# Optimization experiments

Hardware: AMD Instinct MI355X
Metric: run time of the kernel (lower is better)

## Reference

```python
import jax, jax.numpy as jnp
import numpy as np

D = 256
H = 256
B = 128
T = 512


def _init_cell(key, input_size, hidden_size):
    K = 1.0 / np.sqrt(hidden_size)
    k1, k2, k3, k4 = jax.random.split(key, 4)
    u = lambda k, shape: jax.random.uniform(k, shape, jnp.float32, -K, K)
    return (u(k1, (3 * hidden_size, input_size)),
            u(k2, (3 * hidden_size, hidden_size)),
            u(k3, (3 * hidden_size,)),
            u(k4, (3 * hidden_size,)))


def setup_inputs() -> dict:
    key = jax.random.key(0)
    kx, kf, kb = jax.random.split(key, 3)
    x = jax.random.normal(kx, (B, T, D), dtype=jnp.float32)
    w_ih_fw, w_hh_fw, b_ih_fw, b_hh_fw = _init_cell(kf, D, H)
    w_ih_bw, w_hh_bw, b_ih_bw, b_hh_bw = _init_cell(kb, D, H)
    return {
        "x": x,
        "w_ih_fw": w_ih_fw, "w_hh_fw": w_hh_fw, "b_ih_fw": b_ih_fw, "b_hh_fw": b_hh_fw,
        "w_ih_bw": w_ih_bw, "w_hh_bw": w_hh_bw, "b_ih_bw": b_ih_bw, "b_hh_bw": b_hh_bw,
    }


def _gru_scan(x_tbd, w_ih, w_hh, b_ih, b_hh):
    # x_tbd: [T, B, D]; returns outputs [T, B, H] and final h [B, H]
    h0 = jnp.zeros((x_tbd.shape[1], H), dtype=x_tbd.dtype)

    def step(h, x_t):
        xT = x_t @ w_ih.T + b_ih          # [B, 3H]
        hT = h @ w_hh.T + b_hh            # [B, 3H]
        s = jax.nn.sigmoid(xT + hT)
        r = s[:, :H]
        z = s[:, H:2 * H]
        n = jnp.tanh(xT[:, 2 * H:] + r * hT[:, 2 * H:])
        h_new = (1.0 - z) * n + z * h
        return h_new, h_new

    h_last, outs = jax.lax.scan(step, h0, x_tbd)
    return outs, h_last


def reference(x, w_ih_fw, w_hh_fw, b_ih_fw, b_hh_fw,
              w_ih_bw, w_hh_bw, b_ih_bw, b_hh_bw):
    x_tbd = jnp.swapaxes(x, 0, 1)                         # [T, B, D]
    outs_fw, h_fw = _gru_scan(x_tbd, w_ih_fw, w_hh_fw, b_ih_fw, b_hh_fw)
    outs_bw_rev, h_bw = _gru_scan(x_tbd[::-1], w_ih_bw, w_hh_bw, b_ih_bw, b_hh_bw)
    outs_bw = outs_bw_rev[::-1]
    outputs = jnp.concatenate([outs_fw, outs_bw], axis=-1)  # [T, B, 2H]
    outputs = jnp.swapaxes(outputs, 0, 1)                   # [B, T, 2H]
    return outputs, h_fw, h_bw
```

## Files before the change

kernel.cpp:

```cpp
#include <hip/hip_runtime.h>
#include <stdint.h>
#include <stddef.h>

#define T_ 512
#define B_ 128
#define D_ 256
#define H_ 256
#define NR 768
#define OUT_MAIN 33554432ull
#define XT_STRIDE 12288
#define HB 280

typedef __attribute__((ext_vector_type(4))) float f32x4;
typedef __attribute__((ext_vector_type(8))) short s16x8;

__device__ __forceinline__ unsigned short f2bf(float f) {
    union { float f; uint32_t u; } v; v.f = f;
    return (unsigned short)((v.u + 0x7FFFu + ((v.u >> 16) & 1u)) >> 16);
}
__device__ __forceinline__ float bf2f(unsigned short h) {
    union { uint32_t u; float f; } v; v.u = ((uint32_t)h) << 16;
    return v.f;
}
__device__ __forceinline__ float sigm(float x) {
    return __builtin_amdgcn_rcpf(1.f + __expf(-x));
}
__device__ __forceinline__ float tanh_(float x) {
    float e = __expf(2.f * x);
    return 1.f - 2.f * __builtin_amdgcn_rcpf(e + 1.f);
}
__device__ __forceinline__ s16x8 pack8(const float* f) {
    union { s16x8 v; unsigned short u[8]; } p;
#pragma unroll
    for (int i = 0; i < 8; ++i) p.u[i] = f2bf(f[i]);
    return p.v;
}

__global__ void k_convert(const float* __restrict__ wf, const float* __restrict__ wb,
                          unsigned short* __restrict__ dst) {
    int i = blockIdx.x * blockDim.x + threadIdx.x;
    const int n = NR * D_;
    if (i < n) dst[i] = f2bf(wf[i]);
    else if (i < 2 * n) dst[i] = f2bf(wb[i - n]);
}

__global__ __launch_bounds__(512, 2) void k_xgemm(
    const float* __restrict__ x, const unsigned short* __restrict__ wbf,
    const float* __restrict__ bih_f, const float* __restrict__ bhh_f,
    const float* __restrict__ bih_b, const float* __restrict__ bhh_b,
    unsigned short* __restrict__ XT)
{
    __shared__ __align__(16) unsigned short lds_a[64 * 72];
    const int tid = threadIdx.x;
    const int lane = tid & 63, wn = tid >> 6;
    const int t = blockIdx.x;
    const int dir = blockIdx.y >> 1, mh = blockIdx.y & 1;

    f32x4 acc[4][6];
#pragma unroll
    for (int m = 0; m < 4; ++m)
#pragma unroll
        for (int n = 0; n < 6; ++n) acc[m][n] = (f32x4){0.f, 0.f, 0.f, 0.f};

    for (int kb = 0; kb < 4; ++kb) {
        if (kb) __syncthreads();
        {
            int row = tid >> 3, seg = tid & 7;
            const float* src = x + ((size_t)(mh * 64 + row) * T_ + t) * D_ + kb * 64 + seg * 8;
            float fv[8];
            *(f32x4*)&fv[0] = *(const f32x4*)(src);
            *(f32x4*)&fv[4] = *(const f32x4*)(src + 4);
            *(s16x8*)&lds_a[row * 72 + seg * 8] = pack8(fv);
        }
        __syncthreads();
#pragma unroll
        for (int kt = 0; kt < 2; ++kt) {
            s16x8 av[4];
#pragma unroll
            for (int mt = 0; mt < 4; ++mt) {
                int r = mt * 16 + (lane & 15);
                av[mt] = *(const s16x8*)&lds_a[r * 72 + kt * 32 + (lane >> 4) * 8];
            }
#pragma unroll
            for (int nt = 0; nt < 6; ++nt) {
                int c = dir * NR + wn * 96 + nt * 16 + (lane & 15);
                s16x8 bv = *(const s16x8*)(wbf + (size_t)c * D_ + kb * 64 + kt * 32 + (lane >> 4) * 8);
#pragma unroll
                for (int mt = 0; mt < 4; ++mt)
                    acc[mt][nt] = __builtin_amdgcn_mfma_f32_16x16x32_bf16(av[mt], bv, acc[mt][nt], 0, 0, 0);
            }
        }
    }
    const float* bih = dir ? bih_b : bih_f;
    const float* bhh = dir ? bhh_b : bhh_f;
#pragma unroll
    for (int nt = 0; nt < 6; ++nt) {
        const int cw = wn * 96 + nt * 16 + (lane & 15);
        const int gate = cw >> 8, j = cw & 255;
        const int jt = (j >> 4) & 1;
        const int rtid = (j >> 5) * 64 + (((lane >> 4)) << 4) + (j & 15);
        float bias = bih[cw] + (cw < 512 ? bhh[cw] : 0.f);
#pragma unroll
        for (int mt = 0; mt < 4; ++mt) {
#pragma unroll
            for (int q = 0; q < 4; ++q) {
                int rr = mh * 64 + mt * 16 + (lane >> 4) * 4 + q;
                int bgrp = rr >> 4;
                int v = (jt * 4 + q) * 3 + gate;
                XT[((size_t)(dir * 8 + bgrp) * T_ + t) * XT_STRIDE + (size_t)rtid * 24 + v]
                    = f2bf(acc[mt][nt][q] + bias);
            }
        }
    }
}

template<int P>
__device__ __forceinline__ void gru_step(
    int s, int dir, int b0, int tid, int lane, int wid,
    const unsigned short* __restrict__ XTw, float* __restrict__ out,
    unsigned short* hb, const s16x8 (&fB)[6][8], float bhn0, float bhn1,
    s16x8 (&CUR)[3], s16x8 (&NXT)[3])
{
    const int t  = dir ? (T_ - 1 - s) : s;
    const int sn = (s < T_ - 1) ? s + 1 : s;
    const int tn = dir ? (T_ - 1 - sn) : sn;
    {
        const s16x8* p = (const s16x8*)(XTw + (size_t)tn * XT_STRIDE) + (size_t)tid * 3;
        NXT[0] = p[0]; NXT[1] = p[1]; NXT[2] = p[2];
    }
    const unsigned short* hr = hb + P * (16 * HB);
    unsigned short*       hw = hb + (P ^ 1) * (16 * HB);

    f32x4 acc[6];
#pragma unroll
    for (int n = 0; n < 6; ++n) acc[n] = (f32x4){0.f, 0.f, 0.f, 0.f};
#pragma unroll
    for (int k0 = 0; k0 < 8; ++k0) {
        s16x8 a = *(const s16x8*)&hr[(lane & 15) * HB + k0 * 32 + (lane >> 4) * 8];
#pragma unroll
        for (int nt = 0; nt < 6; ++nt)
            acc[nt] = __builtin_amdgcn_mfma_f32_16x16x32_bf16(a, fB[nt][k0], acc[nt], 0, 0, 0);
    }
#pragma unroll
    for (int jt = 0; jt < 2; ++jt) {
        const int j = 32 * wid + jt * 16 + (lane & 15);
        const float bn = jt ? bhn1 : bhn0;
#pragma unroll
        for (int q = 0; q < 4; ++q) {
            const int row = (lane >> 4) * 4 + q;
            const int v = (jt * 4 + q) * 3;
            float xr = bf2f((unsigned short)CUR[(v + 0) >> 3][(v + 0) & 7]);
            float xz = bf2f((unsigned short)CUR[(v + 1) >> 3][(v + 1) & 7]);
            float xn = bf2f((unsigned short)CUR[(v + 2) >> 3][(v + 2) & 7]);
            float hv = bf2f(hr[row * HB + j]);
            float rg = sigm(acc[jt][q] + xr);
            float zg = sigm(acc[2 + jt][q] + xz);
            float ng = tanh_(xn + rg * (acc[4 + jt][q] + bn));
            float hnew = ng + zg * (hv - ng);
            hw[row * HB + j] = f2bf(hnew);
            size_t off = ((size_t)(b0 + row) << 18) + ((size_t)t << 9) + (size_t)dir * 256 + j;
            out[off] = hnew;
            if (s == T_ - 1)
                out[OUT_MAIN + (size_t)dir * B_ * H_ + (size_t)(b0 + row) * H_ + j] = hnew;
        }
    }
    __builtin_amdgcn_sched_barrier(0);
    asm volatile("s_waitcnt lgkmcnt(0)");
    __builtin_amdgcn_s_barrier();
    __builtin_amdgcn_sched_barrier(0);
}

__global__ __launch_bounds__(512, 2) void k_recur(
    const float* __restrict__ whh_f, const float* __restrict__ whh_b,
    const float* __restrict__ bhh_f, const float* __restrict__ bhh_b,
    const unsigned short* __restrict__ XT,
    float* __restrict__ out)
{
    __shared__ __align__(16) unsigned short hb[2 * 16 * HB];
    const int tid = threadIdx.x, lane = tid & 63, wid = tid >> 6;
    const int bid = blockIdx.x;
    const int dir = bid >> 3, b0 = (bid & 7) * 16;
    const float* whh = dir ? whh_b : whh_f;
    const float* bhh = dir ? bhh_b : bhh_f;

    s16x8 fB[6][8];
#pragma unroll
    for (int g = 0; g < 3; ++g) {
#pragma unroll
        for (int half = 0; half < 2; ++half) {
            int nt = 2 * g + half;
            int cb = g * 256 + 32 * wid + half * 16;
#pragma unroll
            for (int k0 = 0; k0 < 8; ++k0) {
                const float* sp = whh + (size_t)(cb + (lane & 15)) * H_ + k0 * 32 + (lane >> 4) * 8;
                float fv[8];
                *(f32x4*)&fv[0] = *(const f32x4*)(sp);
                *(f32x4*)&fv[4] = *(const f32x4*)(sp + 4);
                fB[nt][k0] = pack8(fv);
            }
        }
    }
    const float bhn0 = bhh[512 + 32 * wid + (lane & 15)];
    const float bhn1 = bhh[512 + 32 * wid + 16 + (lane & 15)];

    for (int i = tid; i < 16 * HB / 2; i += 512) ((uint32_t*)hb)[i] = 0;
    __syncthreads();

    const unsigned short* XTw = XT + (size_t)(dir * 8 + (bid & 7)) * T_ * XT_STRIDE;
    s16x8 XA[3], XB[3];
    {
        const int t0 = dir ? (T_ - 1) : 0;
        const s16x8* p = (const s16x8*)(XTw + (size_t)t0 * XT_STRIDE) + (size_t)tid * 3;
        XA[0] = p[0]; XA[1] = p[1]; XA[2] = p[2];
    }
#pragma unroll 1
    for (int s = 0; s < T_; s += 2) {
        gru_step<0>(s,     dir, b0, tid, lane, wid, XTw, out, hb, fB, bhn0, bhn1, XA, XB);
        gru_step<1>(s + 1, dir, b0, tid, lane, wid, XTw, out, hb, fB, bhn0, bhn1, XB, XA);
    }
}

extern "C" void kernel_launch(void* const* d_in, const int* in_sizes, int n_in,
                              void* d_out, int out_size, void* d_ws, size_t ws_size,
                              hipStream_t stream) {
    const float* x     = (const float*)d_in[0];
    const float* wih_f = (const float*)d_in[1];
    const float* whh_f = (const float*)d_in[2];
    const float* bih_f = (const float*)d_in[3];
    const float* bhh_f = (const float*)d_in[4];
    const float* wih_b = (const float*)d_in[5];
    const float* whh_b = (const float*)d_in[6];
    const float* bih_b = (const float*)d_in[7];
    const float* bhh_b = (const float*)d_in[8];
    float* out = (float*)d_out;

    unsigned short* wbf = (unsigned short*)d_ws;
    unsigned short* XT  = (unsigned short*)((char*)d_ws + 786432);

    k_convert<<<dim3(768), dim3(512), 0, stream>>>(wih_f, wih_b, wbf);
    k_xgemm<<<dim3(512, 4), dim3(512), 0, stream>>>(x, wbf, bih_f, bhh_f, bih_b, bhh_b, XT);
    k_recur<<<dim3(16), dim3(512), 0, stream>>>(whh_f, whh_b, bhh_f, bhh_b, XT, out);
}
```

Before: 1.695 ms.

## Retile input GEMM to 128 rows and streamline recurrent step addressing

The input-projection GEMM now gives each block all 128 batch rows and a 384-column slice, with 8 waves split 2x4. Each weight fragment is therefore fetched once for all rows instead of once per 64-row half. In the recurrent kernel, output offsets are precomputed per thread, XT words are unpacked via 32-bit lanes, and the bf16 conversion uses the hardware v_cvt_pk_bf16_f32 instruction. This trims per-step ALU and address work on the serial critical path. The bf16 rounding now comes from the hardware instruction instead of the hand-written routine, so results could differ slightly.

```diff
diff --git a/kernel.cpp b/kernel.cpp
--- a/kernel.cpp
+++ b/kernel.cpp
@@ -13,6 +13,7 @@
 
 typedef __attribute__((ext_vector_type(4))) float f32x4;
 typedef __attribute__((ext_vector_type(8))) short s16x8;
+typedef __attribute__((ext_vector_type(4))) uint32_t u32x4;
 
 __device__ __forceinline__ unsigned short f2bf(float f) {
     union { float f; uint32_t u; } v; v.f = f;
@@ -21,6 +22,17 @@
 __device__ __forceinline__ float bf2f(unsigned short h) {
     union { uint32_t u; float f; } v; v.u = ((uint32_t)h) << 16;
     return v.f;
+}
+__device__ __forceinline__ float lo16(uint32_t w) {
+    union { uint32_t u; float f; } v; v.u = w << 16; return v.f;
+}
+__device__ __forceinline__ float hi16(uint32_t w) {
+    union { uint32_t u; float f; } v; v.u = w & 0xffff0000u; return v.f;
+}
+__device__ __forceinline__ uint32_t cvt1bf(float x) {
+    uint32_t r;
+    asm("v_cvt_pk_bf16_f32 %0, %1, %2" : "=v"(r) : "v"(x), "v"(x));
+    return r;
 }
 __device__ __forceinline__ float sigm(float x) {
     return __builtin_amdgcn_rcpf(1.f + __expf(-x));
@@ -50,11 +62,12 @@
     const float* __restrict__ bih_b, const float* __restrict__ bhh_b,
     unsigned short* __restrict__ XT)
 {
-    __shared__ __align__(16) unsigned short lds_a[64 * 72];
+    __shared__ __align__(16) unsigned short lds_a[128 * 72];
     const int tid = threadIdx.x;
-    const int lane = tid & 63, wn = tid >> 6;
+    const int lane = tid & 63, wid = tid >> 6;
+    const int wm = wid >> 2, wn = wid & 3;
     const int t = blockIdx.x;
-    const int dir = blockIdx.y >> 1, mh = blockIdx.y & 1;
+    const int cblk = blockIdx.y * 384;
 
     f32x4 acc[4][6];
 #pragma unroll
@@ -65,12 +78,15 @@
     for (int kb = 0; kb < 4; ++kb) {
         if (kb) __syncthreads();
         {
-            int row = tid >> 3, seg = tid & 7;
-            const float* src = x + ((size_t)(mh * 64 + row) * T_ + t) * D_ + kb * 64 + seg * 8;
-            float fv[8];
-            *(f32x4*)&fv[0] = *(const f32x4*)(src);
-            *(f32x4*)&fv[4] = *(const f32x4*)(src + 4);
-            *(s16x8*)&lds_a[row * 72 + seg * 8] = pack8(fv);
+            int row = tid >> 2, seg = tid & 3;
+            const float* src = x + ((size_t)row * T_ + t) * D_ + kb * 64 + seg * 16;
+            float fv[16];
+            *(f32x4*)&fv[0]  = *(const f32x4*)(src);
+            *(f32x4*)&fv[4]  = *(const f32x4*)(src + 4);
+            *(f32x4*)&fv[8]  = *(const f32x4*)(src + 8);
+            *(f32x4*)&fv[12] = *(const f32x4*)(src + 12);
+            *(s16x8*)&lds_a[row * 72 + seg * 16]     = pack8(&fv[0]);
+            *(s16x8*)&lds_a[row * 72 + seg * 16 + 8] = pack8(&fv[8]);
         }
         __syncthreads();
 #pragma unroll
@@ -78,37 +94,39 @@
             s16x8 av[4];
 #pragma unroll
             for (int mt = 0; mt < 4; ++mt) {
-                int r = mt * 16 + (lane & 15);
+                int r = wm * 64 + mt * 16 + (lane & 15);
                 av[mt] = *(const s16x8*)&lds_a[r * 72 + kt * 32 + (lane >> 4) * 8];
             }
 #pragma unroll
             for (int nt = 0; nt < 6; ++nt) {
-                int c = dir * NR + wn * 96 + nt * 16 + (lane & 15);
-                s16x8 bv = *(const s16x8*)(wbf + (size_t)c * D_ + kb * 64 + kt * 32 + (lane >> 4) * 8);
+                int c = cblk + wn * 96 + nt * 16 + (lane & 15);
+                const unsigned short* bs = wbf + (size_t)c * D_ + kb * 64 + kt * 32 + (lane >> 4) * 8;
+                s16x8 bv = *(const s16x8*)bs;
 #pragma unroll
                 for (int mt = 0; mt < 4; ++mt)
                     acc[mt][nt] = __builtin_amdgcn_mfma_f32_16x16x32_bf16(av[mt], bv, acc[mt][nt], 0, 0, 0);
             }
         }
     }
+    const int dir = blockIdx.y >> 1;
     const float* bih = dir ? bih_b : bih_f;
     const float* bhh = dir ? bhh_b : bhh_f;
 #pragma unroll
     for (int nt = 0; nt < 6; ++nt) {
-        const int cw = wn * 96 + nt * 16 + (lane & 15);
+        const int cw = (blockIdx.y & 1) * 384 + wn * 96 + nt * 16 + (lane & 15);
         const int gate = cw >> 8, j = cw & 255;
         const int jt = (j >> 4) & 1;
-        const int rtid = (j >> 5) * 64 + (((lane >> 4)) << 4) + (j & 15);
+        const int wl = (j >> 5) * 64 + (j & 15);
         float bias = bih[cw] + (cw < 512 ? bhh[cw] : 0.f);
 #pragma unroll
         for (int mt = 0; mt < 4; ++mt) {
 #pragma unroll
             for (int q = 0; q < 4; ++q) {
-                int rr = mh * 64 + mt * 16 + (lane >> 4) * 4 + q;
-                int bgrp = rr >> 4;
-                int v = (jt * 4 + q) * 3 + gate;
-                XT[((size_t)(dir * 8 + bgrp) * T_ + t) * XT_STRIDE + (size_t)rtid * 24 + v]
-                    = f2bf(acc[mt][nt][q] + bias);
+                int rr = wm * 64 + mt * 16 + (lane >> 4) * 4 + q;
+                int tid_r = wl + (((rr & 15) >> 2) << 4);
+                size_t idx = ((size_t)(dir * 8 + (rr >> 4)) * T_ + t) * XT_STRIDE
+                           + (size_t)tid_r * 24 + (size_t)((jt * 4 + q) * 3 + gate);
+                XT[idx] = f2bf(acc[mt][nt][q] + bias);
             }
         }
     }
@@ -119,14 +137,14 @@
     int s, int dir, int b0, int tid, int lane, int wid,
     const unsigned short* __restrict__ XTw, float* __restrict__ out,
     unsigned short* hb, const s16x8 (&fB)[6][8], float bhn0, float bhn1,
-    s16x8 (&CUR)[3], s16x8 (&NXT)[3])
+    u32x4 (&CUR)[3], u32x4 (&NXT)[3], const uint32_t (&ooff)[2][4])
 {
     const int t  = dir ? (T_ - 1 - s) : s;
     const int sn = (s < T_ - 1) ? s + 1 : s;
     const int tn = dir ? (T_ - 1 - sn) : sn;
     {
-        const s16x8* p = (const s16x8*)(XTw + (size_t)tn * XT_STRIDE) + (size_t)tid * 3;
-        NXT[0] = p[0]; NXT[1] = p[1]; NXT[2] = p[2];
+        const u32x4* p = (const u32x4*)(XTw + (size_t)tn * XT_STRIDE);
+        NXT[0] = p[tid * 3]; NXT[1] = p[tid * 3 + 1]; NXT[2] = p[tid * 3 + 2];
     }
     const unsigned short* hr = hb + P * (16 * HB);
     unsigned short*       hw = hb + (P ^ 1) * (16 * HB);
@@ -141,6 +159,8 @@
         for (int nt = 0; nt < 6; ++nt)
             acc[nt] = __builtin_amdgcn_mfma_f32_16x16x32_bf16(a, fB[nt][k0], acc[nt], 0, 0, 0);
     }
+
+    float* outT = out + ((size_t)t << 9);
 #pragma unroll
     for (int jt = 0; jt < 2; ++jt) {
         const int j = 32 * wid + jt * 16 + (lane & 15);
@@ -149,17 +169,19 @@
         for (int q = 0; q < 4; ++q) {
             const int row = (lane >> 4) * 4 + q;
             const int v = (jt * 4 + q) * 3;
-            float xr = bf2f((unsigned short)CUR[(v + 0) >> 3][(v + 0) & 7]);
-            float xz = bf2f((unsigned short)CUR[(v + 1) >> 3][(v + 1) & 7]);
-            float xn = bf2f((unsigned short)CUR[(v + 2) >> 3][(v + 2) & 7]);
+            uint32_t w0 = CUR[(v)     >> 3][((v)     >> 1) & 3];
+            uint32_t w1 = CUR[(v + 1) >> 3][((v + 1) >> 1) & 3];
+            uint32_t w2 = CUR[(v + 2) >> 3][((v + 2) >> 1) & 3];
+            float xr = (v & 1)       ? hi16(w0) : lo16(w0);
+            float xz = ((v + 1) & 1) ? hi16(w1) : lo16(w1);
+            float xn = ((v + 2) & 1) ? hi16(w2) : lo16(w2);
             float hv = bf2f(hr[row * HB + j]);
             float rg = sigm(acc[jt][q] + xr);
             float zg = sigm(acc[2 + jt][q] + xz);
             float ng = tanh_(xn + rg * (acc[4 + jt][q] + bn));
             float hnew = ng + zg * (hv - ng);
-            hw[row * HB + j] = f2bf(hnew);
-            size_t off = ((size_t)(b0 + row) << 18) + ((size_t)t << 9) + (size_t)dir * 256 + j;
-            out[off] = hnew;
+            hw[row * HB + j] = (unsigned short)cvt1bf(hnew);
+            *(float*)((char*)outT + ooff[jt][q]) = hnew;
             if (s == T_ - 1)
                 out[OUT_MAIN + (size_t)dir * B_ * H_ + (size_t)(b0 + row) * H_ + j] = hnew;
         }
@@ -203,20 +225,31 @@
     const float bhn0 = bhh[512 + 32 * wid + (lane & 15)];
     const float bhn1 = bhh[512 + 32 * wid + 16 + (lane & 15)];
 
+    uint32_t ooff[2][4];
+#pragma unroll
+    for (int jt = 0; jt < 2; ++jt)
+#pragma unroll
+        for (int q = 0; q < 4; ++q) {
+            const int row = (lane >> 4) * 4 + q;
+            const int j = 32 * wid + jt * 16 + (lane & 15);
+            ooff[jt][q] = (uint32_t)(((((uint32_t)(b0 + row)) << 18)
+                                      + (uint32_t)dir * 256u + (uint32_t)j) * 4u);
+        }
+
     for (int i = tid; i < 16 * HB / 2; i += 512) ((uint32_t*)hb)[i] = 0;
     __syncthreads();
 
-    const unsigned short* XTw = XT + (size_t)(dir * 8 + (bid & 7)) * T_ * XT_STRIDE;
-    s16x8 XA[3], XB[3];
+    const unsigned short* XTw = XT + (size_t)bid * T_ * XT_STRIDE;
+    u32x4 XA[3], XB[3];
     {
         const int t0 = dir ? (T_ - 1) : 0;
-        const s16x8* p = (const s16x8*)(XTw + (size_t)t0 * XT_STRIDE) + (size_t)tid * 3;
-        XA[0] = p[0]; XA[1] = p[1]; XA[2] = p[2];
+        const u32x4* p = (const u32x4*)(XTw + (size_t)t0 * XT_STRIDE);
+        XA[0] = p[tid * 3]; XA[1] = p[tid * 3 + 1]; XA[2] = p[tid * 3 + 2];
     }
 #pragma unroll 1
     for (int s = 0; s < T_; s += 2) {
-        gru_step<0>(s,     dir, b0, tid, lane, wid, XTw, out, hb, fB, bhn0, bhn1, XA, XB);
-        gru_step<1>(s + 1, dir, b0, tid, lane, wid, XTw, out, hb, fB, bhn0, bhn1, XB, XA);
+        gru_step<0>(s,     dir, b0, tid, lane, wid, XTw, out, hb, fB, bhn0, bhn1, XA, XB, ooff);
+        gru_step<1>(s + 1, dir, b0, tid, lane, wid, XTw, out, hb, fB, bhn0, bhn1, XB, XA, ooff);
     }
 }
 
```

After: 2.017 ms. 19.0% more time.
